# Kernel tuning notes

Hardware: AMD Instinct MI355X
Metric: run time of the kernel (lower is better)

Reference implementation:

```python
import jax, jax.numpy as jnp
import numpy as np

DA, DZ, HID, IM = 5, 10, 128, 64


def _encode(x, w1, b1, w2, b2, w3, b3, wd, bd):
    # Conv2D k=4 s=2 'same' (pad 1,1) + ReLU, x3, then flatten + Dense(20)
    dn = ('NHWC', 'HWIO', 'NHWC')
    for w, b in ((w1, b1), (w2, b2), (w3, b3)):
        x = jax.lax.conv_general_dilated(x, w, (2, 2), [(1, 1), (1, 1)], dimension_numbers=dn)
        x = jax.nn.relu(x + b)
    x = x.reshape(x.shape[0], -1)
    return x @ wd + bd


def _lstm(a_in, k, rk, b):
    # keras LSTM, gate order i,f,c,o; stateful step-by-step == scan over shifted seq
    B = a_in.shape[0]
    def step(carry, x):
        h, c = carry
        g = x @ k + h @ rk + b
        gi, gf, gg, go = jnp.split(g, 4, axis=-1)
        c = jax.nn.sigmoid(gf) * c + jax.nn.sigmoid(gi) * jnp.tanh(gg)
        h = jax.nn.sigmoid(go) * jnp.tanh(c)
        return (h, c), h
    z = jnp.zeros((B, HID), a_in.dtype)
    _, hs = jax.lax.scan(step, (z, z), jnp.swapaxes(a_in, 0, 1))
    return hs  # [T, B, HID]


def _forward(images, w1, b1, w2, b2, w3, b3, wd, bd, lk, lrk, lb, wabc, babc):
    B, T = images.shape[0], images.shape[1]
    # encode all frames in one batched pass (per-frame encode is recursion-independent)
    lat = _encode(images.reshape(B * T, IM, IM, 1), w1, b1, w2, b2, w3, b3, wd, bd)
    a_all = lat[:, :DA].reshape(B, T, DA)  # encode() mean split
    # LSTM consumes a_prev: a0=zeros at t=0, then a_{t-1}
    a_in = jnp.concatenate([jnp.zeros((B, 1, DA), a_all.dtype), a_all[:, :-1]], axis=1)
    hs = _lstm(a_in, lk, lrk, lb)  # [T,B,HID]
    abc = hs @ wabc + babc  # [T,B,DZ*DZ+DA*DZ]
    A = abc[..., :DZ * DZ].reshape(T, B, DZ, DZ)
    C = abc[..., DZ * DZ:].reshape(T, B, DA, DZ)

    Q = 0.08 * jnp.eye(DZ, dtype=a_all.dtype)
    R = 0.03 * jnp.eye(DA, dtype=a_all.dtype)
    I = jnp.eye(DZ, dtype=a_all.dtype)
    std_min = 1e-4 * I

    def kf(carry, inp):
        z, P = carry
        At, Ct, at = inp
        z_hat = jnp.einsum('bij,bj->bi', At, z)
        P_hat = At @ P @ jnp.swapaxes(At, -1, -2) + Q
        resid = at - jnp.einsum('bij,bj->bi', Ct, z_hat)
        S = Ct @ P_hat @ jnp.swapaxes(Ct, -1, -2) + R
        K = P_hat @ jnp.swapaxes(Ct, -1, -2) @ jnp.linalg.inv(S)
        pz = z_hat + jnp.einsum('bij,bj->bi', K, resid)
        pP = (I - K @ Ct) @ P_hat
        # note: clamped P_hat is stored, but update() above used the unclamped one
        return (pz, pP), (z_hat, jnp.maximum(P_hat, std_min), pz, pP)

    z0 = jnp.zeros((B, DZ), a_all.dtype)
    P0 = jnp.broadcast_to(I, (B, DZ, DZ))
    _, (z_hat_s, P_hat_s, pz_s, pP_s) = jax.lax.scan(kf, (z0, P0), (A, C, jnp.swapaxes(a_all, 0, 1)))
    last_z, last_P = pz_s[-1], pP_s[-1]

    def rts(carry, inp):
        zs, Ps = carry
        pz_prev, pP_prev, Aj, zhj, Phj = inp
        D = pP_prev @ jnp.swapaxes(Aj, -1, -2) @ jnp.linalg.inv(Phj)
        zn = pz_prev + jnp.einsum('bij,bj->bi', D, zs - zhj)
        Pn = pP_prev + D @ (Ps - Phj) @ jnp.swapaxes(D, -1, -2)
        return (zn, Pn), (zn, Pn)

    # j = T-1 .. 1, reading post[j-1], A[j], z_hat[j], P_hat_clamped[j]
    rev = (pz_s[:-1][::-1], pP_s[:-1][::-1], A[1:][::-1], z_hat_s[1:][::-1], P_hat_s[1:][::-1])
    _, (zsm_r, Psm_r) = jax.lax.scan(rts, (last_z, last_P), rev)
    z_smooth = jnp.swapaxes(zsm_r[::-1], 0, 1)  # [B, T-1, DZ]
    P_smooth = jnp.swapaxes(Psm_r[::-1], 0, 1)  # [B, T-1, DZ, DZ]
    return z_smooth, P_smooth, a_all, A, C, last_z, last_P


def setup_inputs() -> dict:
    key = jax.random.key(0)
    ks = jax.random.split(key, 9)
    B, T = 3, 128
    f = lambda k, shape, s: jax.random.normal(k, shape, jnp.float32) * s
    return {
        'images': jax.random.uniform(ks[0], (B, T, IM, IM, 1), jnp.float32),
        'w1': f(ks[1], (4, 4, 1, 64), 0.25), 'b1': jnp.zeros((64,), jnp.float32),
        'w2': f(ks[2], (4, 4, 64, 128), 0.03), 'b2': jnp.zeros((128,), jnp.float32),
        'w3': f(ks[3], (4, 4, 128, 512), 0.022), 'b3': jnp.zeros((512,), jnp.float32),
        'wd': f(ks[4], (8 * 8 * 512, 20), 0.006), 'bd': jnp.zeros((20,), jnp.float32),
        'lk': f(ks[5], (DA, 4 * HID), 0.3), 'lrk': f(ks[6], (HID, 4 * HID), 0.08),
        'lb': jnp.zeros((4 * HID,), jnp.float32),
        'wabc': f(ks[7], (HID, DZ * DZ + DA * DZ), 0.02),
        'babc': jnp.zeros((DZ * DZ + DA * DZ,), jnp.float32),
    }


def reference(images, w1, b1, w2, b2, w3, b3, wd, bd, lk, lrk, lb, wabc, babc):
    return _forward(images, w1, b1, w2, b2, w3, b3, wd, bd, lk, lrk, lb, wabc, babc)
```

## Files before the change

### kernel.cpp

```cpp
#include <hip/hip_runtime.h>
#include <math.h>

typedef unsigned int   u32;
typedef unsigned short u16;
typedef short bf16x8 __attribute__((ext_vector_type(8)));
typedef float f32x4  __attribute__((ext_vector_type(4)));

#define OUT_ZS    0
#define OUT_PS    3810
#define OUT_AALL  41910
#define OUT_A     43830
#define OUT_C     82230
#define OUT_LASTZ 101430
#define OUT_LASTP 101460

__device__ __forceinline__ float sigm(float x){ return 1.f/(1.f+expf(-x)); }
__device__ __forceinline__ float safed(float d){
    return (fabsf(d) < 1e-30f) ? ((d < 0.f) ? -1e-30f : 1e-30f) : d;
}
__device__ __forceinline__ u16 f2b(float f) {
    union { float f; u32 u; } v; v.f = f;
    u32 r = v.u + 0x7fffu + ((v.u >> 16) & 1u);
    return (u16)(r >> 16);
}
__device__ __forceinline__ float b2f(u16 u) {
    union { u32 x; float f; } v; v.x = ((u32)u) << 16; return v.f;
}
__device__ __forceinline__ u32 packb(float a, float b){ return (u32)f2b(a) | ((u32)f2b(b) << 16); }

__device__ u16   r14_c1[25165824];
__device__ u16   r14_c2[12582912];
__device__ float r14_c3[12582912];
__device__ u16   r14_w2h[131072];
__device__ u16   r14_w2l[131072];
__device__ u16   r14_w3h[1048576];
__device__ u16   r14_w3l[1048576];
__device__ float r14_wdT[163840];
__device__ float r14_hs[49152];
__device__ float r14_zhat[3840];
__device__ float r14_phat[38400];
__device__ float r14_pz[3840];
__device__ float r14_pp[38400];
__device__ float r14_aall[1920];
__device__ float r14_A[38400];
__device__ float r14_C[19200];
__device__ float r14_G[38400];

__global__ __launch_bounds__(256) void conv1_r14(const float* __restrict__ img,
        const float* __restrict__ w1, const float* __restrict__ b1, u16* __restrict__ out)
{
    __shared__ float in_lds[66*66];
    const int f = blockIdx.x, tid = threadIdx.x;
    const int og = tid >> 5, sg = tid & 31;

    for (int i = tid; i < 66*66; i += 256) in_lds[i] = 0.f;
    __syncthreads();
    const float4* src = (const float4*)(img + f*4096);
    for (int i = tid; i < 1024; i += 256) {
        int r = i >> 4, c0 = (i & 15) * 4;
        float4 v = src[i];
        float* dst = &in_lds[(r+1)*66 + c0 + 1];
        dst[0]=v.x; dst[1]=v.y; dst[2]=v.z; dst[3]=v.w;
    }
    float wr[16][8];
    #pragma unroll
    for (int k = 0; k < 16; k++) {
        float4 a = *(const float4*)&w1[k*64 + og*8];
        float4 b = *(const float4*)&w1[k*64 + og*8 + 4];
        wr[k][0]=a.x; wr[k][1]=a.y; wr[k][2]=a.z; wr[k][3]=a.w;
        wr[k][4]=b.x; wr[k][5]=b.y; wr[k][6]=b.z; wr[k][7]=b.w;
    }
    float bias[8];
    #pragma unroll
    for (int j = 0; j < 8; j++) bias[j] = b1[og*8+j];
    __syncthreads();

    for (int yy = 0; yy < 32; yy++) {
        float inv[16];
        #pragma unroll
        for (int ky = 0; ky < 4; ky++)
            #pragma unroll
            for (int kx = 0; kx < 4; kx++)
                inv[ky*4+kx] = in_lds[(2*yy+ky)*66 + 2*sg+kx];
        float acc[8];
        #pragma unroll
        for (int j = 0; j < 8; j++) acc[j] = bias[j];
        #pragma unroll
        for (int k = 0; k < 16; k++)
            #pragma unroll
            for (int j = 0; j < 8; j++) acc[j] += inv[k]*wr[k][j];
        #pragma unroll
        for (int j = 0; j < 8; j++) acc[j] = fmaxf(acc[j], 0.f);
        uint4 pk = make_uint4(packb(acc[0],acc[1]), packb(acc[2],acc[3]),
                              packb(acc[4],acc[5]), packb(acc[6],acc[7]));
        *(uint4*)(out + (f*1024 + yy*32 + sg)*64 + og*8) = pk;
    }
}

__global__ __launch_bounds__(256) void w2t_r14(const float* __restrict__ w2,
        u16* __restrict__ hi, u16* __restrict__ lo)
{
    int idx = blockIdx.x*256 + threadIdx.x;
    if (idx < 131072) {
        int k = idx >> 7, oc = idx & 127;
        float v = w2[idx];
        u16 h = f2b(v);
        hi[oc*1024 + k] = h;
        lo[oc*1024 + k] = f2b(v - b2f(h));
    }
}
__global__ __launch_bounds__(256) void w3t_r14(const float* __restrict__ w3,
        u16* __restrict__ hi, u16* __restrict__ lo)
{
    int idx = blockIdx.x*256 + threadIdx.x;
    if (idx < 1048576) {
        int k = idx >> 9, oc = idx & 511;
        float v = w3[idx];
        u16 h = f2b(v);
        hi[oc*2048 + k] = h;
        lo[oc*2048 + k] = f2b(v - b2f(h));
    }
}
__global__ __launch_bounds__(256) void wdt_r14(const float* __restrict__ wd, float* __restrict__ wdT)
{
    int idx = blockIdx.x*256 + threadIdx.x;
    if (idx < 163840) {
        int j = idx & 32767, d = idx >> 15;
        wdT[d*32768 + j] = wd[j*20 + d];
    }
}

__global__ __launch_bounds__(256) void conv2_r14(const u16* __restrict__ c1b,
        const u16* __restrict__ w2h, const u16* __restrict__ w2l,
        const float* __restrict__ b2, u16* __restrict__ c2b)
{
    __shared__ __align__(16) u16 slab[128*72];
    const int f = blockIdx.x, mc = blockIdx.y, tid = threadIdx.x;
    const int wave = tid >> 6, lane = tid & 63, quad = lane >> 4, ln = lane & 15;

    f32x4 acc[8][2];
    const f32x4 zz = {0.f, 0.f, 0.f, 0.f};
    #pragma unroll
    for (int mt = 0; mt < 8; mt++) { acc[mt][0] = zz; acc[mt][1] = zz; }

    const int sp = tid >> 1;
    const int sy = mc*8 + (sp >> 4), sx = sp & 15;
    const int sic = (tid & 1) * 32;

    for (int kk = 0; kk < 16; kk++) {
        const int ky = kk >> 2, kx = kk & 3;
        __syncthreads();
        {
            int iy = 2*sy - 1 + ky, ix = 2*sx - 1 + kx;
            uint4* d4 = (uint4*)&slab[sp*72 + sic];
            if (iy >= 0 && iy < 32 && ix >= 0 && ix < 32) {
                const uint4* s4 = (const uint4*)&c1b[((f*32 + iy)*32 + ix)*64 + sic];
                d4[0]=s4[0]; d4[1]=s4[1]; d4[2]=s4[2]; d4[3]=s4[3];
            } else {
                uint4 z = make_uint4(0,0,0,0);
                d4[0]=z; d4[1]=z; d4[2]=z; d4[3]=z;
            }
        }
        __syncthreads();
        #pragma unroll
        for (int ks = 0; ks < 2; ks++) {
            bf16x8 af[8];
            #pragma unroll
            for (int mt = 0; mt < 8; mt++)
                af[mt] = *(const bf16x8*)&slab[(mt*16 + ln)*72 + ks*32 + quad*8];
            #pragma unroll
            for (int nt = 0; nt < 2; nt++) {
                const int oc = wave*32 + nt*16 + ln;
                const int kb = kk*64 + ks*32 + quad*8;
                bf16x8 bh = *(const bf16x8*)&w2h[oc*1024 + kb];
                bf16x8 bl = *(const bf16x8*)&w2l[oc*1024 + kb];
                #pragma unroll
                for (int mt = 0; mt < 8; mt++) {
                    acc[mt][nt] = __builtin_amdgcn_mfma_f32_16x16x32_bf16(af[mt], bh, acc[mt][nt], 0,0,0);
                    acc[mt][nt] = __builtin_amdgcn_mfma_f32_16x16x32_bf16(af[mt], bl, acc[mt][nt], 0,0,0);
                }
            }
        }
    }
    #pragma unroll
    for (int nt = 0; nt < 2; nt++) {
        const int oc = wave*32 + nt*16 + ln;
        const float bias = b2[oc];
        #pragma unroll
        for (int mt = 0; mt < 8; mt++)
            #pragma unroll
            for (int r = 0; r < 4; r++) {
                int pix = mc*128 + mt*16 + quad*4 + r;
                c2b[(f*256 + pix)*128 + oc] = f2b(fmaxf(acc[mt][nt][r] + bias, 0.f));
            }
    }
}

__global__ __launch_bounds__(256) void conv3_r14(const u16* __restrict__ c2b,
        const u16* __restrict__ w3h, const u16* __restrict__ w3l,
        const float* __restrict__ b3, float* __restrict__ c3)
{
    __shared__ __align__(16) u16 slab[64*136];
    const int f = blockIdx.x, ocg = blockIdx.y, tid = threadIdx.x;
    const int wave = tid >> 6, lane = tid & 63, quad = lane >> 4, ln = lane & 15;
    const int wn = ocg*256 + wave*64;

    f32x4 acc[4][4];
    const f32x4 zz = {0.f, 0.f, 0.f, 0.f};
    #pragma unroll
    for (int mt = 0; mt < 4; mt++)
        #pragma unroll
        for (int nt = 0; nt < 4; nt++) acc[mt][nt] = zz;

    const int sp = tid >> 2;
    const int sy = sp >> 3, sx = sp & 7;
    const int sic = (tid & 3) * 32;

    for (int kk = 0; kk < 16; kk++) {
        const int ky = kk >> 2, kx = kk & 3;
        __syncthreads();
        {
            int iy = 2*sy - 1 + ky, ix = 2*sx - 1 + kx;
            uint4* d4 = (uint4*)&slab[sp*136 + sic];
            if (iy >= 0 && iy < 16 && ix >= 0 && ix < 16) {
                const uint4* s4 = (const uint4*)&c2b[((f*16 + iy)*16 + ix)*128 + sic];
                d4[0]=s4[0]; d4[1]=s4[1]; d4[2]=s4[2]; d4[3]=s4[3];
            } else {
                uint4 z = make_uint4(0,0,0,0);
                d4[0]=z; d4[1]=z; d4[2]=z; d4[3]=z;
            }
        }
        __syncthreads();
        #pragma unroll
        for (int ks = 0; ks < 4; ks++) {
            bf16x8 af[4];
            #pragma unroll
            for (int mt = 0; mt < 4; mt++)
                af[mt] = *(const bf16x8*)&slab[(mt*16 + ln)*136 + ks*32 + quad*8];
            #pragma unroll
            for (int nt = 0; nt < 4; nt++) {
                const int oc = wn + nt*16 + ln;
                const int kb = kk*128 + ks*32 + quad*8;
                bf16x8 bh = *(const bf16x8*)&w3h[oc*2048 + kb];
                bf16x8 bl = *(const bf16x8*)&w3l[oc*2048 + kb];
                #pragma unroll
                for (int mt = 0; mt < 4; mt++) {
                    acc[mt][nt] = __builtin_amdgcn_mfma_f32_16x16x32_bf16(af[mt], bh, acc[mt][nt], 0,0,0);
                    acc[mt][nt] = __builtin_amdgcn_mfma_f32_16x16x32_bf16(af[mt], bl, acc[mt][nt], 0,0,0);
                }
            }
        }
    }
    #pragma unroll
    for (int nt = 0; nt < 4; nt++) {
        const int oc = wn + nt*16 + ln;
        const float bias = b3[oc];
        #pragma unroll
        for (int mt = 0; mt < 4; mt++)
            #pragma unroll
            for (int r = 0; r < 4; r++) {
                int pix = mt*16 + quad*4 + r;
                c3[(f*64 + pix)*512 + oc] = fmaxf(acc[mt][nt][r] + bias, 0.f);
            }
    }
}

__global__ __launch_bounds__(256) void dense_r14(const float* __restrict__ bd,
        float* __restrict__ dout)
{
    const int f = blockIdx.x, tid = threadIdx.x;
    float p0=0,p1=0,p2=0,p3=0,p4=0;
    const float4* x4 = (const float4*)(r14_c3 + f*32768);
    for (int j = tid; j < 8192; j += 256) {
        float4 v = x4[j];
        float4 w0 = *(const float4*)&r14_wdT[          4*j];
        float4 w1 = *(const float4*)&r14_wdT[32768   + 4*j];
        float4 w2 = *(const float4*)&r14_wdT[65536   + 4*j];
        float4 w3 = *(const float4*)&r14_wdT[98304   + 4*j];
        float4 w4 = *(const float4*)&r14_wdT[131072  + 4*j];
        p0 += v.x*w0.x + v.y*w0.y + v.z*w0.z + v.w*w0.w;
        p1 += v.x*w1.x + v.y*w1.y + v.z*w1.z + v.w*w1.w;
        p2 += v.x*w2.x + v.y*w2.y + v.z*w2.z + v.w*w2.w;
        p3 += v.x*w3.x + v.y*w3.y + v.z*w3.z + v.w*w3.w;
        p4 += v.x*w4.x + v.y*w4.y + v.z*w4.z + v.w*w4.w;
    }
    __shared__ float red[5][256];
    red[0][tid]=p0; red[1][tid]=p1; red[2][tid]=p2; red[3][tid]=p3; red[4][tid]=p4;
    __syncthreads();
    for (int st = 128; st > 0; st >>= 1) {
        if (tid < st) {
            #pragma unroll
            for (int d = 0; d < 5; d++) red[d][tid] += red[d][tid+st];
        }
        __syncthreads();
    }
    if (tid < 5) {
        float v = red[tid][0] + bd[tid];
        r14_aall[f*5 + tid] = v;
        dout[OUT_AALL + f*5 + tid] = v;
    }
}

__global__ __launch_bounds__(512) void lstm_r14(const float* __restrict__ lk,
        const float* __restrict__ lrk, const float* __restrict__ lb)
{
    const int b = blockIdx.x, c = threadIdx.x;
    __shared__ float a_lds[640];
    __shared__ float h_lds[128];
    __shared__ float g_lds[512];
    for (int i = c; i < 640; i += 512) a_lds[i] = r14_aall[b*640 + i];
    if (c < 128) h_lds[c] = 0.f;
    float wreg[128];
    #pragma unroll
    for (int j = 0; j < 128; j++) wreg[j] = lrk[j*512 + c];
    float lkr[5];
    #pragma unroll
    for (int d = 0; d < 5; d++) lkr[d] = lk[d*512 + c];
    const float gb = lb[c];
    float cs = 0.f;
    __syncthreads();
    for (int t = 0; t < 128; t++) {
        float g = gb;
        if (t > 0) {
            #pragma unroll
            for (int d = 0; d < 5; d++) g += a_lds[(t-1)*5 + d] * lkr[d];
        }
        float s0=0.f, s1=0.f, s2=0.f, s3=0.f;
        #pragma unroll
        for (int j = 0; j < 128; j += 4) {
            float4 h4 = *(const float4*)&h_lds[j];
            s0 += h4.x*wreg[j];   s1 += h4.y*wreg[j+1];
            s2 += h4.z*wreg[j+2]; s3 += h4.w*wreg[j+3];
        }
        g += (s0 + s1) + (s2 + s3);
        g_lds[c] = g;
        __syncthreads();
        if (c < 128) {
            float gi = g_lds[c], gf = g_lds[c+128], gg = g_lds[c+256], go = g_lds[c+384];
            cs = sigm(gf)*cs + sigm(gi)*tanhf(gg);
            float hn = sigm(go)*tanhf(cs);
            h_lds[c] = hn;
            r14_hs[(t*3 + b)*128 + c] = hn;
        }
        __syncthreads();
    }
}

__global__ __launch_bounds__(192) void abc_r14(const float* __restrict__ wabc,
        const float* __restrict__ babc, float* __restrict__ dout)
{
    const int tb = blockIdx.x, c = threadIdx.x;
    __shared__ float h_lds[128];
    if (c < 128) h_lds[c] = r14_hs[tb*128 + c];
    __syncthreads();
    if (c < 150) {
        float s = babc[c];
        for (int j = 0; j < 128; j++) s += h_lds[j]*wabc[j*150 + c];
        if (c < 100) { r14_A[tb*100 + c] = s; dout[OUT_A + tb*100 + c] = s; }
        else         { r14_C[tb*50 + (c-100)] = s; dout[OUT_C + tb*50 + (c-100)] = s; }
    }
}

__global__ __launch_bounds__(128) void kf_r15(float* __restrict__ dout)
{
    const int b = blockIdx.x, tid = threadIdx.x;
    const int i10 = tid/10, j10 = tid%10;
    __shared__ float Ab[2][100], Cb[2][56], avb[2][8];
    __shared__ float z[12], P[100], zh[12], AP[100], Ph[100], resid[8],
                     CPm[52], PCt[52], Ssh[28], Kg[52];

    float rA = 0.f, rC = 0.f, rav = 0.f;
    if (tid < 100) rA  = r14_A[(0*3+b)*100 + tid];
    if (tid < 50)  rC  = r14_C[(0*3+b)*50 + tid];
    if (tid < 5)   rav = r14_aall[(b*128+0)*5 + tid];
    if (tid < 100) P[tid] = (i10==j10) ? 1.f : 0.f;
    if (tid < 10)  z[tid] = 0.f;
    if (tid < 100) Ab[0][tid] = rA;
    if (tid < 50)  Cb[0][tid] = rC;
    if (tid < 5)   avb[0][tid] = rav;
    if (tid < 100) rA  = r14_A[(1*3+b)*100 + tid];
    if (tid < 50)  rC  = r14_C[(1*3+b)*50 + tid];
    if (tid < 5)   rav = r14_aall[(b*128+1)*5 + tid];
    __syncthreads();

    for (int t = 0; t < 128; t++) {
        const int cb = t & 1, nb = cb ^ 1;
        const float* Ax = Ab[cb];
        const float* Cx = Cb[cb];

        if (tid < 100) {
            float s = 0.f;
            #pragma unroll
            for (int k = 0; k < 10; k++) s += Ax[i10*10+k]*P[k*10+j10];
            AP[tid] = s;
        } else if (tid < 110) {
            const int i = tid - 100;
            float s = 0.f;
            #pragma unroll
            for (int k = 0; k < 10; k++) s += Ax[i*10+k]*z[k];
            zh[i] = s;
        }
        __syncthreads();

        if (tid < 100) {
            float s = (i10==j10) ? 0.08f : 0.f;
            #pragma unroll
            for (int k = 0; k < 10; k++) s += AP[i10*10+k]*Ax[j10*10+k];
            Ph[tid] = s;
        } else if (tid < 105) {
            const int c = tid - 100;
            float s = avb[cb][c];
            #pragma unroll
            for (int k = 0; k < 10; k++) s -= Cx[c*10+k]*zh[k];
            resid[c] = s;
        }
        __syncthreads();

        if (tid < 50) {
            const int i = tid/10, j = tid%10;
            float s = 0.f;
            #pragma unroll
            for (int k = 0; k < 10; k++) s += Cx[i*10+k]*Ph[k*10+j];
            CPm[tid] = s;
        } else if (tid >= 64 && tid < 114) {
            const int q = tid-64, i = q/5, j = q%5;
            float s = 0.f;
            #pragma unroll
            for (int k = 0; k < 10; k++) s += Ph[i*10+k]*Cx[j*10+k];
            PCt[q] = s;
        }
        __syncthreads();

        if (tid < 25) {
            const int i = tid/5, j = tid%5;
            float s = (i==j) ? 0.03f : 0.f;
            #pragma unroll
            for (int k = 0; k < 10; k++) s += CPm[i*10+k]*Cx[j*10+k];
            Ssh[tid] = s;
        }
        __syncthreads();

        if (tid < 10) {
            float M[5][5], bb[5], pv[5], x[5];
            #pragma unroll
            for (int r = 0; r < 5; r++)
                #pragma unroll
                for (int c = 0; c < 5; c++) M[r][c] = Ssh[c*5+r];
            #pragma unroll
            for (int k = 0; k < 5; k++) bb[k] = PCt[tid*5+k];
            #pragma unroll
            for (int k = 0; k < 5; k++) {
                const float p = 1.f/safed(M[k][k]);
                pv[k] = p;
                #pragma unroll
                for (int r = k+1; r < 5; r++) {
                    const float f = M[r][k]*p;
                    #pragma unroll
                    for (int c = k+1; c < 5; c++) M[r][c] -= f*M[k][c];
                    bb[r] -= f*bb[k];
                }
            }
            #pragma unroll
            for (int k = 4; k >= 0; k--) {
                float s = bb[k];
                #pragma unroll
                for (int c = k+1; c < 5; c++) s -= M[k][c]*x[c];
                x[k] = s*pv[k];
            }
            #pragma unroll
            for (int k = 0; k < 5; k++) Kg[tid*5+k] = x[k];
        }
        __syncthreads();

        if (tid < 100) {
            float s = Ph[tid];
            #pragma unroll
            for (int k = 0; k < 5; k++) s -= Kg[i10*5+k]*CPm[k*10+j10];
            r14_pp[(t*3+b)*100 + tid] = s;
            P[tid] = s;
            r14_phat[(t*3+b)*100 + tid] = fmaxf(Ph[tid], (i10==j10)?1e-4f:0.f);
            if (tid < 10) r14_zhat[(t*3+b)*10 + tid] = zh[tid];
        } else if (tid < 110) {
            const int i = tid - 100;
            float s = zh[i];
            #pragma unroll
            for (int k = 0; k < 5; k++) s += Kg[i*5+k]*resid[k];
            r14_pz[(t*3+b)*10 + i] = s;
            z[i] = s;
        }
        if (t < 127) {
            if (tid < 100) Ab[nb][tid] = rA;
            if (tid < 50)  Cb[nb][tid] = rC;
            if (tid < 5)   avb[nb][tid] = rav;
            if (t < 126) {
                if (tid < 100) rA  = r14_A[((t+2)*3+b)*100 + tid];
                if (tid < 50)  rC  = r14_C[((t+2)*3+b)*50 + tid];
                if (tid < 5)   rav = r14_aall[(b*128+(t+2))*5 + tid];
            }
        }
        __syncthreads();
    }
    if (tid < 10)  dout[OUT_LASTZ + b*10 + tid]  = z[tid];
    if (tid < 100) dout[OUT_LASTP + b*100 + tid] = P[tid];
}

__global__ __launch_bounds__(256) void ginv_r14()
{
    const int idx = blockIdx.x;
    const int tt = idx/3 + 1, b = idx%3;
    const int tid = threadIdx.x;
    __shared__ float M[10][21];
    __shared__ float A[100];
    __shared__ int piv;
    if (tid < 100) {
        int i = tid/10, j = tid%10;
        M[i][j] = r14_phat[(tt*3+b)*100 + tid];
        M[i][10+j] = (i==j) ? 1.f : 0.f;
        A[tid] = r14_A[(tt*3+b)*100 + tid];
    }
    __syncthreads();
    const int r = tid/20, cc = tid%20;
    for (int k = 0; k < 10; k++) {
        if (tid == 0) {
            int p = k; float best = fabsf(M[k][k]);
            for (int rr = k+1; rr < 10; rr++) {
                float v = fabsf(M[rr][k]);
                if (v > best) { best = v; p = rr; }
            }
            piv = p;
        }
        __syncthreads();
        if (piv != k && tid < 20) {
            float a = M[k][tid], bb = M[piv][tid];
            M[k][tid] = bb; M[piv][tid] = a;
        }
        __syncthreads();
        float pinv = 1.f/safed(M[k][k]);
        float myf = 0.f, rowv = 0.f;
        if (tid < 200) { myf = M[r][k]; rowv = M[k][cc]; }
        __syncthreads();
        if (tid < 200) {
            if (r == k) M[k][cc] = rowv*pinv;
            else        M[r][cc] -= myf*pinv*rowv;
        }
        __syncthreads();
    }
    if (tid < 100) {
        int i = tid/10, j = tid%10;
        float s = 0.f;
        #pragma unroll
        for (int k = 0; k < 10; k++) s += A[k*10+i]*M[k][10+j];
        r14_G[(tt*3+b)*100 + tid] = s;
    }
}

__global__ __launch_bounds__(128) void rts_r14(float* __restrict__ dout)
{
    const int b = blockIdx.x, tid = threadIdx.x;
    const int i10 = tid/10, j10 = tid%10;
    __shared__ float zc[10], Pc[100], D[100], Gt[100], pPm[100], ph[100],
                     zh[10], pzv[10], dz[10], T1[100], zn[10], Pnn[100];
    if (tid < 10)  zc[tid] = r14_pz[(127*3+b)*10 + tid];
    if (tid < 100) Pc[tid] = r14_pp[(127*3+b)*100 + tid];
    for (int t = 126; t >= 0; t--) {
        __syncthreads();
        if (tid < 100) {
            Gt[tid]  = r14_G[((t+1)*3+b)*100 + tid];
            pPm[tid] = r14_pp[(t*3+b)*100 + tid];
            ph[tid]  = r14_phat[((t+1)*3+b)*100 + tid];
        }
        if (tid < 10) {
            zh[tid]  = r14_zhat[((t+1)*3+b)*10 + tid];
            pzv[tid] = r14_pz[(t*3+b)*10 + tid];
        }
        __syncthreads();
        if (tid < 100){ float s=0.f; for (int k=0;k<10;k++) s += pPm[i10*10+k]*Gt[k*10+j10]; D[tid]=s; }
        if (tid < 10) dz[tid] = zc[tid] - zh[tid];
        __syncthreads();
        if (tid < 10) { float s=pzv[tid]; for (int k=0;k<10;k++) s += D[tid*10+k]*dz[k]; zn[tid]=s; }
        if (tid < 100){ float s=0.f; for (int k=0;k<10;k++) s += D[i10*10+k]*(Pc[k*10+j10]-ph[k*10+j10]); T1[tid]=s; }
        __syncthreads();
        if (tid < 100){ float s=pPm[tid]; for (int k=0;k<10;k++) s += T1[i10*10+k]*D[j10*10+k]; Pnn[tid]=s; }
        __syncthreads();
        if (tid < 10) { dout[OUT_ZS + (b*127+t)*10 + tid] = zn[tid]; zc[tid]=zn[tid]; }
        if (tid < 100){ dout[OUT_PS + (b*127+t)*100 + tid] = Pnn[tid]; Pc[tid]=Pnn[tid]; }
    }
}

extern "C" void kernel_launch(void* const* d_in, const int* in_sizes, int n_in,
                              void* d_out, int out_size, void* d_ws, size_t ws_size,
                              hipStream_t stream)
{
    (void)in_sizes; (void)n_in; (void)out_size; (void)d_ws; (void)ws_size;
    const float* images = (const float*)d_in[0];
    const float* w1   = (const float*)d_in[1];
    const float* b1   = (const float*)d_in[2];
    const float* w2   = (const float*)d_in[3];
    const float* b2   = (const float*)d_in[4];
    const float* w3   = (const float*)d_in[5];
    const float* b3   = (const float*)d_in[6];
    const float* wd   = (const float*)d_in[7];
    const float* bd   = (const float*)d_in[8];
    const float* lk   = (const float*)d_in[9];
    const float* lrk  = (const float*)d_in[10];
    const float* lb   = (const float*)d_in[11];
    const float* wabc = (const float*)d_in[12];
    const float* babc = (const float*)d_in[13];
    float* dout = (float*)d_out;

    u16 *c1p, *c2p, *w2hp, *w2lp, *w3hp, *w3lp;
    float *c3p, *wdTp;
    hipGetSymbolAddress((void**)&c1p,  HIP_SYMBOL(r14_c1));
    hipGetSymbolAddress((void**)&c2p,  HIP_SYMBOL(r14_c2));
    hipGetSymbolAddress((void**)&c3p,  HIP_SYMBOL(r14_c3));
    hipGetSymbolAddress((void**)&w2hp, HIP_SYMBOL(r14_w2h));
    hipGetSymbolAddress((void**)&w2lp, HIP_SYMBOL(r14_w2l));
    hipGetSymbolAddress((void**)&w3hp, HIP_SYMBOL(r14_w3h));
    hipGetSymbolAddress((void**)&w3lp, HIP_SYMBOL(r14_w3l));
    hipGetSymbolAddress((void**)&wdTp, HIP_SYMBOL(r14_wdT));

    conv1_r14<<<dim3(384), dim3(256), 0, stream>>>(images, w1, b1, c1p);
    w2t_r14<<<dim3(512), dim3(256), 0, stream>>>(w2, w2hp, w2lp);
    w3t_r14<<<dim3(4096), dim3(256), 0, stream>>>(w3, w3hp, w3lp);
    wdt_r14<<<dim3(640), dim3(256), 0, stream>>>(wd, wdTp);
    conv2_r14<<<dim3(384, 2), dim3(256), 0, stream>>>(c1p, w2hp, w2lp, b2, c2p);
    conv3_r14<<<dim3(384, 2), dim3(256), 0, stream>>>(c2p, w3hp, w3lp, b3, c3p);
    dense_r14<<<dim3(384), dim3(256), 0, stream>>>(bd, dout);
    lstm_r14<<<dim3(3), dim3(512), 0, stream>>>(lk, lrk, lb);
    abc_r14<<<dim3(384), dim3(192), 0, stream>>>(wabc, babc, dout);
    kf_r15<<<dim3(3), dim3(128), 0, stream>>>(dout);
    ginv_r14<<<dim3(381), dim3(256), 0, stream>>>();
    rts_r14<<<dim3(3), dim3(128), 0, stream>>>(dout);
}
```

Before: 1.008 ms.

## Fuse dense into conv3 epilogue and shrink KF/RTS kernels to one wave

The dense projection is folded into the conv3 epilogue. Each block multiplies its ReLU outputs by the wd rows directly, reduces them in LDS, and writes a partial sum, so the 50MB c3 intermediate, the wd transpose kernel and the separate dense kernel all go away. The LSTM kernel now sums the two partials plus bias to build a_all. The Kalman filter and RTS smoother are rewritten to use a single 64-thread wave, with each thread handling up to two matrix elements. RTS additionally double-buffers its per-step loads in registers, cutting barrier cost and exposed global latency on the serial chain. The risk is uncoalesced strided wd reads (stride of 20 floats) in the conv3 epilogue.

Result: slower. 1.102 ms (+9.3%).

```diff
diff --git a/kernel.cpp b/kernel.cpp
--- a/kernel.cpp
+++ b/kernel.cpp
@@ -30,12 +30,11 @@
 
 __device__ u16   r14_c1[25165824];
 __device__ u16   r14_c2[12582912];
-__device__ float r14_c3[12582912];
 __device__ u16   r14_w2h[131072];
 __device__ u16   r14_w2l[131072];
 __device__ u16   r14_w3h[1048576];
 __device__ u16   r14_w3l[1048576];
-__device__ float r14_wdT[163840];
+__device__ float r20_dpart[3840];
 __device__ float r14_hs[49152];
 __device__ float r14_zhat[3840];
 __device__ float r14_phat[38400];
@@ -121,14 +120,6 @@
         lo[oc*2048 + k] = f2b(v - b2f(h));
     }
 }
-__global__ __launch_bounds__(256) void wdt_r14(const float* __restrict__ wd, float* __restrict__ wdT)
-{
-    int idx = blockIdx.x*256 + threadIdx.x;
-    if (idx < 163840) {
-        int j = idx & 32767, d = idx >> 15;
-        wdT[d*32768 + j] = wd[j*20 + d];
-    }
-}
 
 __global__ __launch_bounds__(256) void conv2_r14(const u16* __restrict__ c1b,
         const u16* __restrict__ w2h, const u16* __restrict__ w2l,
@@ -196,9 +187,9 @@
     }
 }
 
-__global__ __launch_bounds__(256) void conv3_r14(const u16* __restrict__ c2b,
+__global__ __launch_bounds__(256) void conv3_r20(const u16* __restrict__ c2b,
         const u16* __restrict__ w3h, const u16* __restrict__ w3l,
-        const float* __restrict__ b3, float* __restrict__ c3)
+        const float* __restrict__ b3, const float* __restrict__ wd)
 {
     __shared__ __align__(16) u16 slab[64*136];
     const int f = blockIdx.x, ocg = blockIdx.y, tid = threadIdx.x;
@@ -251,6 +242,8 @@
             }
         }
     }
+
+    float pd0=0.f, pd1=0.f, pd2=0.f, pd3=0.f, pd4=0.f;
     #pragma unroll
     for (int nt = 0; nt < 4; nt++) {
         const int oc = wn + nt*16 + ln;
@@ -259,56 +252,44 @@
         for (int mt = 0; mt < 4; mt++)
             #pragma unroll
             for (int r = 0; r < 4; r++) {
-                int pix = mt*16 + quad*4 + r;
-                c3[(f*64 + pix)*512 + oc] = fmaxf(acc[mt][nt][r] + bias, 0.f);
-            }
-    }
-}
-
-__global__ __launch_bounds__(256) void dense_r14(const float* __restrict__ bd,
-        float* __restrict__ dout)
-{
-    const int f = blockIdx.x, tid = threadIdx.x;
-    float p0=0,p1=0,p2=0,p3=0,p4=0;
-    const float4* x4 = (const float4*)(r14_c3 + f*32768);
-    for (int j = tid; j < 8192; j += 256) {
-        float4 v = x4[j];
-        float4 w0 = *(const float4*)&r14_wdT[          4*j];
-        float4 w1 = *(const float4*)&r14_wdT[32768   + 4*j];
-        float4 w2 = *(const float4*)&r14_wdT[65536   + 4*j];
-        float4 w3 = *(const float4*)&r14_wdT[98304   + 4*j];
-        float4 w4 = *(const float4*)&r14_wdT[131072  + 4*j];
-        p0 += v.x*w0.x + v.y*w0.y + v.z*w0.z + v.w*w0.w;
-        p1 += v.x*w1.x + v.y*w1.y + v.z*w1.z + v.w*w1.w;
-        p2 += v.x*w2.x + v.y*w2.y + v.z*w2.z + v.w*w2.w;
-        p3 += v.x*w3.x + v.y*w3.y + v.z*w3.z + v.w*w3.w;
-        p4 += v.x*w4.x + v.y*w4.y + v.z*w4.z + v.w*w4.w;
-    }
-    __shared__ float red[5][256];
-    red[0][tid]=p0; red[1][tid]=p1; red[2][tid]=p2; red[3][tid]=p3; red[4][tid]=p4;
+                const int pix = mt*16 + quad*4 + r;
+                const float v = fmaxf(acc[mt][nt][r] + bias, 0.f);
+                const float* wp = &wd[(pix*512 + oc)*20];
+                float4 w4 = *(const float4*)wp;
+                pd0 += v*w4.x; pd1 += v*w4.y; pd2 += v*w4.z; pd3 += v*w4.w;
+                pd4 += v*wp[4];
+            }
+    }
+    __syncthreads();
+    float* red = (float*)slab;
+    red[0*256+tid]=pd0; red[1*256+tid]=pd1; red[2*256+tid]=pd2;
+    red[3*256+tid]=pd3; red[4*256+tid]=pd4;
     __syncthreads();
     for (int st = 128; st > 0; st >>= 1) {
         if (tid < st) {
             #pragma unroll
-            for (int d = 0; d < 5; d++) red[d][tid] += red[d][tid+st];
-        }
-        __syncthreads();
-    }
-    if (tid < 5) {
-        float v = red[tid][0] + bd[tid];
-        r14_aall[f*5 + tid] = v;
-        dout[OUT_AALL + f*5 + tid] = v;
-    }
-}
-
-__global__ __launch_bounds__(512) void lstm_r14(const float* __restrict__ lk,
-        const float* __restrict__ lrk, const float* __restrict__ lb)
+            for (int d = 0; d < 5; d++) red[d*256+tid] += red[d*256+tid+st];
+        }
+        __syncthreads();
+    }
+    if (tid < 5) r20_dpart[(f*2 + ocg)*5 + tid] = red[tid*256];
+}
+
+__global__ __launch_bounds__(512) void lstm_r20(const float* __restrict__ lk,
+        const float* __restrict__ lrk, const float* __restrict__ lb,
+        const float* __restrict__ bd, float* __restrict__ dout)
 {
     const int b = blockIdx.x, c = threadIdx.x;
     __shared__ float a_lds[640];
     __shared__ float h_lds[128];
     __shared__ float g_lds[512];
-    for (int i = c; i < 640; i += 512) a_lds[i] = r14_aall[b*640 + i];
+    for (int i = c; i < 640; i += 512) {
+        const int f = b*128 + i/5, d = i % 5;
+        const float v = bd[d] + r20_dpart[f*10 + d] + r20_dpart[f*10 + 5 + d];
+        a_lds[i] = v;
+        r14_aall[f*5 + d] = v;
+        dout[OUT_AALL + f*5 + d] = v;
+    }
     if (c < 128) h_lds[c] = 0.f;
     float wreg[128];
     #pragma unroll
@@ -361,26 +342,35 @@
     }
 }
 
-__global__ __launch_bounds__(128) void kf_r15(float* __restrict__ dout)
+__global__ __launch_bounds__(64) void kf_r20(float* __restrict__ dout)
 {
     const int b = blockIdx.x, tid = threadIdx.x;
-    const int i10 = tid/10, j10 = tid%10;
+    const int e1 = tid + 64;
+    const int i0 = tid/10, j0 = tid%10;
+    const int i1 = e1/10, j1 = e1%10;
+    const bool h1 = (tid < 36);
+    const bool hz = (tid >= 36 && tid < 46);
+    const int zi = tid - 36;
     __shared__ float Ab[2][100], Cb[2][56], avb[2][8];
     __shared__ float z[12], P[100], zh[12], AP[100], Ph[100], resid[8],
                      CPm[52], PCt[52], Ssh[28], Kg[52];
 
-    float rA = 0.f, rC = 0.f, rav = 0.f;
-    if (tid < 100) rA  = r14_A[(0*3+b)*100 + tid];
-    if (tid < 50)  rC  = r14_C[(0*3+b)*50 + tid];
-    if (tid < 5)   rav = r14_aall[(b*128+0)*5 + tid];
-    if (tid < 100) P[tid] = (i10==j10) ? 1.f : 0.f;
-    if (tid < 10)  z[tid] = 0.f;
-    if (tid < 100) Ab[0][tid] = rA;
-    if (tid < 50)  Cb[0][tid] = rC;
-    if (tid < 5)   avb[0][tid] = rav;
-    if (tid < 100) rA  = r14_A[(1*3+b)*100 + tid];
-    if (tid < 50)  rC  = r14_C[(1*3+b)*50 + tid];
-    if (tid < 5)   rav = r14_aall[(b*128+1)*5 + tid];
+    float rA0 = 0.f, rA1 = 0.f, rC = 0.f, rav = 0.f;
+    rA0 = r14_A[b*100 + tid];
+    if (h1)      rA1 = r14_A[b*100 + e1];
+    if (tid<50)  rC  = r14_C[b*50 + tid];
+    if (tid<5)   rav = r14_aall[(b*128+0)*5 + tid];
+    P[tid] = (i0==j0) ? 1.f : 0.f;
+    if (h1) P[e1] = (i1==j1) ? 1.f : 0.f;
+    if (tid < 10) z[tid] = 0.f;
+    Ab[0][tid] = rA0;
+    if (h1)     Ab[0][e1] = rA1;
+    if (tid<50) Cb[0][tid] = rC;
+    if (tid<5)  avb[0][tid] = rav;
+    rA0 = r14_A[(3+b)*100 + tid];
+    if (h1)      rA1 = r14_A[(3+b)*100 + e1];
+    if (tid<50)  rC  = r14_C[(3+b)*50 + tid];
+    if (tid<5)   rav = r14_aall[(b*128+1)*5 + tid];
     __syncthreads();
 
     for (int t = 0; t < 128; t++) {
@@ -388,46 +378,68 @@
         const float* Ax = Ab[cb];
         const float* Cx = Cb[cb];
 
-        if (tid < 100) {
+        {
             float s = 0.f;
             #pragma unroll
-            for (int k = 0; k < 10; k++) s += Ax[i10*10+k]*P[k*10+j10];
+            for (int k = 0; k < 10; k++) s += Ax[i0*10+k]*P[k*10+j0];
             AP[tid] = s;
-        } else if (tid < 110) {
-            const int i = tid - 100;
-            float s = 0.f;
-            #pragma unroll
-            for (int k = 0; k < 10; k++) s += Ax[i*10+k]*z[k];
-            zh[i] = s;
-        }
-        __syncthreads();
-
-        if (tid < 100) {
-            float s = (i10==j10) ? 0.08f : 0.f;
-            #pragma unroll
-            for (int k = 0; k < 10; k++) s += AP[i10*10+k]*Ax[j10*10+k];
+            if (h1) {
+                float s1 = 0.f;
+                #pragma unroll
+                for (int k = 0; k < 10; k++) s1 += Ax[i1*10+k]*P[k*10+j1];
+                AP[e1] = s1;
+            }
+            if (hz) {
+                float s2 = 0.f;
+                #pragma unroll
+                for (int k = 0; k < 10; k++) s2 += Ax[zi*10+k]*z[k];
+                zh[zi] = s2;
+            }
+        }
+        __syncthreads();
+
+        {
+            float s = (i0==j0) ? 0.08f : 0.f;
+            #pragma unroll
+            for (int k = 0; k < 10; k++) s += AP[i0*10+k]*Ax[j0*10+k];
             Ph[tid] = s;
-        } else if (tid < 105) {
-            const int c = tid - 100;
-            float s = avb[cb][c];
-            #pragma unroll
-            for (int k = 0; k < 10; k++) s -= Cx[c*10+k]*zh[k];
-            resid[c] = s;
-        }
-        __syncthreads();
-
-        if (tid < 50) {
-            const int i = tid/10, j = tid%10;
-            float s = 0.f;
-            #pragma unroll
-            for (int k = 0; k < 10; k++) s += Cx[i*10+k]*Ph[k*10+j];
-            CPm[tid] = s;
-        } else if (tid >= 64 && tid < 114) {
-            const int q = tid-64, i = q/5, j = q%5;
-            float s = 0.f;
-            #pragma unroll
-            for (int k = 0; k < 10; k++) s += Ph[i*10+k]*Cx[j*10+k];
-            PCt[q] = s;
+            if (h1) {
+                float s1 = (i1==j1) ? 0.08f : 0.f;
+                #pragma unroll
+                for (int k = 0; k < 10; k++) s1 += AP[i1*10+k]*Ax[j1*10+k];
+                Ph[e1] = s1;
+            }
+            if (tid >= 36 && tid < 41) {
+                const int c = tid - 36;
+                float s2 = avb[cb][c];
+                #pragma unroll
+                for (int k = 0; k < 10; k++) s2 -= Cx[c*10+k]*zh[k];
+                resid[c] = s2;
+            }
+        }
+        __syncthreads();
+
+        {
+            if (tid < 50) {
+                const int i = tid/10, j = tid%10;
+                float s = 0.f;
+                #pragma unroll
+                for (int k = 0; k < 10; k++) s += Cx[i*10+k]*Ph[k*10+j];
+                CPm[tid] = s;
+            } else {
+                const int q = tid - 50, i = q/5, j = q%5;
+                float s = 0.f;
+                #pragma unroll
+                for (int k = 0; k < 10; k++) s += Ph[i*10+k]*Cx[j*10+k];
+                PCt[q] = s;
+            }
+            if (h1) {
+                const int q = tid + 14, i = q/5, j = q%5;
+                float s = 0.f;
+                #pragma unroll
+                for (int k = 0; k < 10; k++) s += Ph[i*10+k]*Cx[j*10+k];
+                PCt[q] = s;
+            }
         }
         __syncthreads();
 
@@ -472,36 +484,47 @@
         }
         __syncthreads();
 
-        if (tid < 100) {
+        {
             float s = Ph[tid];
             #pragma unroll
-            for (int k = 0; k < 5; k++) s -= Kg[i10*5+k]*CPm[k*10+j10];
+            for (int k = 0; k < 5; k++) s -= Kg[i0*5+k]*CPm[k*10+j0];
             r14_pp[(t*3+b)*100 + tid] = s;
             P[tid] = s;
-            r14_phat[(t*3+b)*100 + tid] = fmaxf(Ph[tid], (i10==j10)?1e-4f:0.f);
+            r14_phat[(t*3+b)*100 + tid] = fmaxf(Ph[tid], (i0==j0)?1e-4f:0.f);
             if (tid < 10) r14_zhat[(t*3+b)*10 + tid] = zh[tid];
-        } else if (tid < 110) {
-            const int i = tid - 100;
-            float s = zh[i];
-            #pragma unroll
-            for (int k = 0; k < 5; k++) s += Kg[i*5+k]*resid[k];
-            r14_pz[(t*3+b)*10 + i] = s;
-            z[i] = s;
-        }
-        if (t < 127) {
-            if (tid < 100) Ab[nb][tid] = rA;
-            if (tid < 50)  Cb[nb][tid] = rC;
-            if (tid < 5)   avb[nb][tid] = rav;
-            if (t < 126) {
-                if (tid < 100) rA  = r14_A[((t+2)*3+b)*100 + tid];
-                if (tid < 50)  rC  = r14_C[((t+2)*3+b)*50 + tid];
-                if (tid < 5)   rav = r14_aall[(b*128+(t+2))*5 + tid];
-            }
-        }
-        __syncthreads();
-    }
-    if (tid < 10)  dout[OUT_LASTZ + b*10 + tid]  = z[tid];
-    if (tid < 100) dout[OUT_LASTP + b*100 + tid] = P[tid];
+            if (h1) {
+                float s1 = Ph[e1];
+                #pragma unroll
+                for (int k = 0; k < 5; k++) s1 -= Kg[i1*5+k]*CPm[k*10+j1];
+                r14_pp[(t*3+b)*100 + e1] = s1;
+                P[e1] = s1;
+                r14_phat[(t*3+b)*100 + e1] = fmaxf(Ph[e1], (i1==j1)?1e-4f:0.f);
+            }
+            if (hz) {
+                float s2 = zh[zi];
+                #pragma unroll
+                for (int k = 0; k < 5; k++) s2 += Kg[zi*5+k]*resid[k];
+                r14_pz[(t*3+b)*10 + zi] = s2;
+                z[zi] = s2;
+            }
+            if (t < 127) {
+                Ab[nb][tid] = rA0;
+                if (h1)     Ab[nb][e1] = rA1;
+                if (tid<50) Cb[nb][tid] = rC;
+                if (tid<5)  avb[nb][tid] = rav;
+                if (t < 126) {
+                    rA0 = r14_A[((t+2)*3+b)*100 + tid];
+                    if (h1)      rA1 = r14_A[((t+2)*3+b)*100 + e1];
+                    if (tid<50)  rC  = r14_C[((t+2)*3+b)*50 + tid];
+                    if (tid<5)   rav = r14_aall[(b*128+(t+2))*5 + tid];
+                }
+            }
+        }
+        __syncthreads();
+    }
+    if (tid < 10) dout[OUT_LASTZ + b*10 + tid] = z[tid];
+    dout[OUT_LASTP + b*100 + tid] = P[tid];
+    if (h1) dout[OUT_LASTP + b*100 + e1] = P[e1];
 }
 
 __global__ __launch_bounds__(256) void ginv_r14()
@@ -554,36 +577,123 @@
     }
 }
 
-__global__ __launch_bounds__(128) void rts_r14(float* __restrict__ dout)
+__global__ __launch_bounds__(64) void rts_r20(float* __restrict__ dout)
 {
     const int b = blockIdx.x, tid = threadIdx.x;
-    const int i10 = tid/10, j10 = tid%10;
-    __shared__ float zc[10], Pc[100], D[100], Gt[100], pPm[100], ph[100],
-                     zh[10], pzv[10], dz[10], T1[100], zn[10], Pnn[100];
-    if (tid < 10)  zc[tid] = r14_pz[(127*3+b)*10 + tid];
-    if (tid < 100) Pc[tid] = r14_pp[(127*3+b)*100 + tid];
+    const int e1 = tid + 64;
+    const int i0 = tid/10, j0 = tid%10;
+    const int i1 = e1/10, j1 = e1%10;
+    const bool h1 = (tid < 36);
+    const bool hz = (tid >= 36 && tid < 46);
+    const int zi = tid - 36;
+    __shared__ float zc[12], Pc[100], D[100], dz[12], T1[100];
+    __shared__ float Gtb[2][100], pPb[2][100], phb[2][100], zhb[2][12], pzb[2][12];
+
+    if (tid < 10) zc[tid] = r14_pz[(127*3+b)*10 + tid];
+    Pc[tid] = r14_pp[(127*3+b)*100 + tid];
+    if (h1) Pc[e1] = r14_pp[(127*3+b)*100 + e1];
+
+    float g0=0.f, g1=0.f, p0=0.f, p1=0.f, f0=0.f, f1=0.f, zr=0.f, pr=0.f;
+    Gtb[0][tid] = r14_G[(127*3+b)*100 + tid];
+    pPb[0][tid] = r14_pp[(126*3+b)*100 + tid];
+    phb[0][tid] = r14_phat[(127*3+b)*100 + tid];
+    if (h1) {
+        Gtb[0][e1] = r14_G[(127*3+b)*100 + e1];
+        pPb[0][e1] = r14_pp[(126*3+b)*100 + e1];
+        phb[0][e1] = r14_phat[(127*3+b)*100 + e1];
+    }
+    if (hz) {
+        zhb[0][zi] = r14_zhat[(127*3+b)*10 + zi];
+        pzb[0][zi] = r14_pz[(126*3+b)*10 + zi];
+    }
+    g0 = r14_G[(126*3+b)*100 + tid];
+    p0 = r14_pp[(125*3+b)*100 + tid];
+    f0 = r14_phat[(126*3+b)*100 + tid];
+    if (h1) {
+        g1 = r14_G[(126*3+b)*100 + e1];
+        p1 = r14_pp[(125*3+b)*100 + e1];
+        f1 = r14_phat[(126*3+b)*100 + e1];
+    }
+    if (hz) {
+        zr = r14_zhat[(126*3+b)*10 + zi];
+        pr = r14_pz[(125*3+b)*10 + zi];
+    }
+    __syncthreads();
+
     for (int t = 126; t >= 0; t--) {
-        __syncthreads();
-        if (tid < 100) {
-            Gt[tid]  = r14_G[((t+1)*3+b)*100 + tid];
-            pPm[tid] = r14_pp[(t*3+b)*100 + tid];
-            ph[tid]  = r14_phat[((t+1)*3+b)*100 + tid];
-        }
-        if (tid < 10) {
-            zh[tid]  = r14_zhat[((t+1)*3+b)*10 + tid];
-            pzv[tid] = r14_pz[(t*3+b)*10 + tid];
-        }
-        __syncthreads();
-        if (tid < 100){ float s=0.f; for (int k=0;k<10;k++) s += pPm[i10*10+k]*Gt[k*10+j10]; D[tid]=s; }
-        if (tid < 10) dz[tid] = zc[tid] - zh[tid];
-        __syncthreads();
-        if (tid < 10) { float s=pzv[tid]; for (int k=0;k<10;k++) s += D[tid*10+k]*dz[k]; zn[tid]=s; }
-        if (tid < 100){ float s=0.f; for (int k=0;k<10;k++) s += D[i10*10+k]*(Pc[k*10+j10]-ph[k*10+j10]); T1[tid]=s; }
-        __syncthreads();
-        if (tid < 100){ float s=pPm[tid]; for (int k=0;k<10;k++) s += T1[i10*10+k]*D[j10*10+k]; Pnn[tid]=s; }
-        __syncthreads();
-        if (tid < 10) { dout[OUT_ZS + (b*127+t)*10 + tid] = zn[tid]; zc[tid]=zn[tid]; }
-        if (tid < 100){ dout[OUT_PS + (b*127+t)*100 + tid] = Pnn[tid]; Pc[tid]=Pnn[tid]; }
+        const int cb = (126 - t) & 1, nb = cb ^ 1;
+
+        {
+            float s = 0.f;
+            #pragma unroll
+            for (int k = 0; k < 10; k++) s += pPb[cb][i0*10+k]*Gtb[cb][k*10+j0];
+            D[tid] = s;
+            if (h1) {
+                float s1 = 0.f;
+                #pragma unroll
+                for (int k = 0; k < 10; k++) s1 += pPb[cb][i1*10+k]*Gtb[cb][k*10+j1];
+                D[e1] = s1;
+            }
+            if (hz) dz[zi] = zc[zi] - zhb[cb][zi];
+        }
+        __syncthreads();
+
+        {
+            float s = 0.f;
+            #pragma unroll
+            for (int k = 0; k < 10; k++) s += D[i0*10+k]*(Pc[k*10+j0] - phb[cb][k*10+j0]);
+            T1[tid] = s;
+            if (h1) {
+                float s1 = 0.f;
+                #pragma unroll
+                for (int k = 0; k < 10; k++) s1 += D[i1*10+k]*(Pc[k*10+j1] - phb[cb][k*10+j1]);
+                T1[e1] = s1;
+            }
+            if (hz) {
+                float s2 = pzb[cb][zi];
+                #pragma unroll
+                for (int k = 0; k < 10; k++) s2 += D[zi*10+k]*dz[k];
+                zc[zi] = s2;
+                dout[OUT_ZS + (b*127+t)*10 + zi] = s2;
+            }
+        }
+        __syncthreads();
+
+        {
+            float s = pPb[cb][tid];
+            #pragma unroll
+            for (int k = 0; k < 10; k++) s += T1[i0*10+k]*D[j0*10+k];
+            dout[OUT_PS + (b*127+t)*100 + tid] = s;
+            Pc[tid] = s;
+            if (h1) {
+                float s1 = pPb[cb][e1];
+                #pragma unroll
+                for (int k = 0; k < 10; k++) s1 += T1[i1*10+k]*D[j1*10+k];
+                dout[OUT_PS + (b*127+t)*100 + e1] = s1;
+                Pc[e1] = s1;
+            }
+            if (t > 0) {
+                Gtb[nb][tid] = g0; pPb[nb][tid] = p0; phb[nb][tid] = f0;
+                if (h1) { Gtb[nb][e1] = g1; pPb[nb][e1] = p1; phb[nb][e1] = f1; }
+                if (hz) { zhb[nb][zi] = zr; pzb[nb][zi] = pr; }
+                if (t > 1) {
+                    const int s2 = t - 2;
+                    g0 = r14_G[((s2+1)*3+b)*100 + tid];
+                    p0 = r14_pp[(s2*3+b)*100 + tid];
+                    f0 = r14_phat[((s2+1)*3+b)*100 + tid];
+                    if (h1) {
+                        g1 = r14_G[((s2+1)*3+b)*100 + e1];
+                        p1 = r14_pp[(s2*3+b)*100 + e1];
+                        f1 = r14_phat[((s2+1)*3+b)*100 + e1];
+                    }
+                    if (hz) {
+                        zr = r14_zhat[((s2+1)*3+b)*10 + zi];
+                        pr = r14_pz[(s2*3+b)*10 + zi];
+                    }
+                }
+            }
+        }
+        __syncthreads();
     }
 }
 
@@ -609,26 +719,21 @@
     float* dout = (float*)d_out;
 
     u16 *c1p, *c2p, *w2hp, *w2lp, *w3hp, *w3lp;
-    float *c3p, *wdTp;
     hipGetSymbolAddress((void**)&c1p,  HIP_SYMBOL(r14_c1));
     hipGetSymbolAddress((void**)&c2p,  HIP_SYMBOL(r14_c2));
-    hipGetSymbolAddress((void**)&c3p,  HIP_SYMBOL(r14_c3));
     hipGetSymbolAddress((void**)&w2hp, HIP_SYMBOL(r14_w2h));
     hipGetSymbolAddress((void**)&w2lp, HIP_SYMBOL(r14_w2l));
     hipGetSymbolAddress((void**)&w3hp, HIP_SYMBOL(r14_w3h));
     hipGetSymbolAddress((void**)&w3lp, HIP_SYMBOL(r14_w3l));
-    hipGetSymbolAddress((void**)&wdTp, HIP_SYMBOL(r14_wdT));
 
     conv1_r14<<<dim3(384), dim3(256), 0, stream>>>(images, w1, b1, c1p);
     w2t_r14<<<dim3(512), dim3(256), 0, stream>>>(w2, w2hp, w2lp);
     w3t_r14<<<dim3(4096), dim3(256), 0, stream>>>(w3, w3hp, w3lp);
-    wdt_r14<<<dim3(640), dim3(256), 0, stream>>>(wd, wdTp);
     conv2_r14<<<dim3(384, 2), dim3(256), 0, stream>>>(c1p, w2hp, w2lp, b2, c2p);
-    conv3_r14<<<dim3(384, 2), dim3(256), 0, stream>>>(c2p, w3hp, w3lp, b3, c3p);
-    dense_r14<<<dim3(384), dim3(256), 0, stream>>>(bd, dout);
-    lstm_r14<<<dim3(3), dim3(512), 0, stream>>>(lk, lrk, lb);
+    conv3_r20<<<dim3(384, 2), dim3(256), 0, stream>>>(c2p, w3hp, w3lp, b3, wd);
+    lstm_r20<<<dim3(3), dim3(512), 0, stream>>>(lk, lrk, lb, bd, dout);
     abc_r14<<<dim3(384), dim3(192), 0, stream>>>(wabc, babc, dout);
-    kf_r15<<<dim3(3), dim3(128), 0, stream>>>(dout);
+    kf_r20<<<dim3(3), dim3(64), 0, stream>>>(dout);
     ginv_r14<<<dim3(381), dim3(256), 0, stream>>>();
-    rts_r14<<<dim3(3), dim3(128), 0, stream>>>(dout);
-}
+    rts_r20<<<dim3(3), dim3(64), 0, stream>>>(dout);
+}
```
